# Optimization experiments

Measured on AMD Instinct MI355X. Metric: run time of the kernel, lower is better.

The kernel has to match this reference:

```python
import jax, jax.numpy as jnp
import numpy as np

NT, NGRID, NX, HID, NY = 365, 1000, 20, 256, 1


def setup_inputs() -> dict:
    key = jax.random.key(0)
    ks = jax.random.split(key, 10)
    s_in = 1.0 / np.sqrt(NX)
    s_h = 1.0 / np.sqrt(HID)
    inp = {
        "x": jax.random.normal(ks[0], (NT, NGRID, NX), dtype=jnp.float32),
        "wt_ih": jnp.zeros((4 * HID, HID), dtype=jnp.float32),
        "W_in": jax.random.uniform(ks[1], (HID, NX), jnp.float32, -s_in, s_in),
        "b_in": jax.random.uniform(ks[2], (HID,), jnp.float32, -s_in, s_in),
        "W_ih": jax.random.uniform(ks[3], (4 * HID, HID), jnp.float32, -s_h, s_h),
        "W_hh": jax.random.uniform(ks[4], (4 * HID, HID), jnp.float32, -s_h, s_h),
        "b_ih": jax.random.uniform(ks[5], (4 * HID,), jnp.float32, -s_h, s_h),
        "b_hh": jax.random.uniform(ks[6], (4 * HID,), jnp.float32, -s_h, s_h),
        "W_out": jax.random.uniform(ks[7], (NY, HID), jnp.float32, -s_h, s_h),
        "b_out": jax.random.uniform(ks[8], (NY,), jnp.float32, -s_h, s_h),
    }
    return inp


def _lstm_forward(x, W_in, b_in, W_ih, W_hh, b_ih, b_hh, W_out, b_out):
    # linearIn + ReLU: [nt, ngrid, hid]
    x0 = jax.nn.relu(jnp.einsum("tnx,hx->tnh", x, W_in) + b_in)
    # precompute input contribution to gates for all timesteps: [nt, ngrid, 4*hid]
    gx = jnp.einsum("tnh,gh->tng", x0, W_ih) + b_ih + b_hh
    h0 = jnp.zeros((x.shape[1], HID), dtype=x.dtype)
    c0 = jnp.zeros((x.shape[1], HID), dtype=x.dtype)

    def step(carry, gx_t):
        h, c = carry
        gates = gx_t + h @ W_hh.T  # [ngrid, 4*hid]
        i, f, g, o = jnp.split(gates, 4, axis=-1)  # torch LSTMCell gate order
        i = jax.nn.sigmoid(i)
        f = jax.nn.sigmoid(f)
        g = jnp.tanh(g)
        o = jax.nn.sigmoid(o)
        c_new = f * c + i * g
        h_new = o * jnp.tanh(c_new)
        return (h_new, c_new), h_new

    _, hs = jax.lax.scan(step, (h0, c0), gx)  # hs: [nt, ngrid, hid]
    return jnp.einsum("tnh,yh->tny", hs, W_out) + b_out


def reference(x, wt_ih, W_in, b_in, W_ih, W_hh, b_ih, b_hh, W_out, b_out):
    # wt_ih only perturbs weights in training mode (and is zero here); eval-mode math:
    return _lstm_forward(x, W_in, b_in, W_ih, W_hh, b_ih, b_hh, W_out, b_out)
```

## Files before the change

### kernel.cpp

```cpp
#include <hip/hip_runtime.h>
#include <hip/hip_fp16.h>

#define NT    365
#define NGRID 1000
#define NXI   20
#define HID   256
#define GATES 1024
#define MROWS 365000
#define MBLK  5704
#define MPAD  (MBLK * 64)
#define NCL   63
#define CPTS  16
#define HX_TOT ((size_t)NT * NCL * 1024)
#define HX_ZERO ((size_t)NCL * 1024)

typedef _Float16 half8 __attribute__((ext_vector_type(8)));
typedef float floatx4 __attribute__((ext_vector_type(4)));
typedef unsigned long long u64;

#define SENT 0xFFFFFFFFFFFFFFFFull

__device__ _Float16 g_gx[(size_t)MPAD * GATES];
__device__ _Float16 g_wif[64 * 8 * 512];
__device__ _Float16 g_whf[2 * 32 * 8 * 64 * 8];
__device__ u64 g_hx[HX_TOT];

__device__ __forceinline__ float fsig(float x) {
  return __fdividef(1.f, 1.f + __expf(-x));
}
__device__ __forceinline__ float ftanh(float x) {
  return 1.f - __fdividef(2.f, __expf(2.f * x) + 1.f);
}

__global__ __launch_bounds__(256) void pack_wf_kernel(
    const float* __restrict__ W_ih, const float* __restrict__ W_hh) {
  const int gid = blockIdx.x * 256 + threadIdx.x;
  const float* src;
  _Float16* dst;
  int n, k0, lane;
  if (gid < 32768) {
    const int tile = gid >> 9;
    const int ks   = (gid >> 6) & 7;
    lane = gid & 63;
    n  = tile * 16 + (lane & 15);
    k0 = ks * 32 + (lane >> 4) * 8;
    src = W_ih + n * HID + k0;
    dst = g_wif + ((size_t)(tile * 8 + ks) * 64 + lane) * 8;
  } else {
    const int rem = gid - 32768;
    const int b2  = rem >> 14;
    const int lt  = (rem >> 9) & 31;
    const int ks  = (rem >> 6) & 7;
    lane = rem & 63;
    const int nt = (lt >> 3) * 16 + b2 * 8 + (lt & 7);
    n  = nt * 16 + (lane & 15);
    k0 = ks * 32 + (lane >> 4) * 8;
    src = W_hh + n * HID + k0;
    dst = g_whf + ((size_t)((b2 * 32 + lt) * 8 + ks) * 64 + lane) * 8;
  }
  const float4 a = *(const float4*)(src);
  const float4 b = *(const float4*)(src + 4);
  half8 h;
  h[0] = (_Float16)a.x; h[1] = (_Float16)a.y; h[2] = (_Float16)a.z; h[3] = (_Float16)a.w;
  h[4] = (_Float16)b.x; h[5] = (_Float16)b.y; h[6] = (_Float16)b.z; h[7] = (_Float16)b.w;
  *(half8*)dst = h;
}

__global__ __launch_bounds__(256, 2) void gx_kernel(
    const float* __restrict__ x, const float* __restrict__ W_in,
    const float* __restrict__ b_in, const float* __restrict__ b_ih,
    const float* __restrict__ b_hh, float* __restrict__ y) {
  {
    const size_t gid = (size_t)blockIdx.x * 256 + threadIdx.x;
    const size_t TT  = (size_t)MBLK * 256;
    for (size_t j = gid; j < HX_TOT; j += TT)
      g_hx[j] = (j < HX_ZERO) ? 0ull : SENT;
    if (gid < MROWS) y[gid] = 0.f;
  }

  __shared__ float s_x[64 * NXI];
  __shared__ float s_bias[GATES];
  __shared__ _Float16 s_x0[64 * 264];
  __shared__ _Float16 s_out[64 * 264];

  const int tid  = threadIdx.x;
  const int lane = tid & 63;
  const int w    = tid >> 6;
  const int jg   = lane >> 4;
  const int m0   = blockIdx.x * 64;

  #pragma unroll
  for (int i = 0; i < 5; ++i) {
    const int idx = i * 256 + tid;
    size_t g = (size_t)m0 * NXI + idx;
    const size_t gmax = (size_t)MROWS * NXI - 1;
    if (g > gmax) g = gmax;
    s_x[idx] = x[g];
  }
  #pragma unroll
  for (int i = 0; i < 4; ++i) {
    const int g = i * 256 + tid;
    s_bias[g] = b_ih[g] + b_hh[g];
  }
  float wv[NXI];
  #pragma unroll
  for (int k = 0; k < NXI; ++k) wv[k] = W_in[tid * NXI + k];
  const float bv = b_in[tid];
  __syncthreads();

  half8 bf[4][4];
  #pragma unroll
  for (int p = 0; p < 4; ++p)
    #pragma unroll
    for (int ni = 0; ni < 4; ++ni)
      bf[p][ni] = *(const half8*)(g_wif +
          ((size_t)((w * 4 + ni) * 8 + p) * 64 + lane) * 8);

  for (int r = 0; r < 64; ++r) {
    float acc = bv;
    #pragma unroll
    for (int qq = 0; qq < 5; ++qq) {
      const float4 xa = *(const float4*)&s_x[r * NXI + qq * 4];
      acc += xa.x * wv[qq * 4 + 0] + xa.y * wv[qq * 4 + 1] +
             xa.z * wv[qq * 4 + 2] + xa.w * wv[qq * 4 + 3];
    }
    s_x0[r * 264 + tid] = (_Float16)fmaxf(acc, 0.f);
  }
  __syncthreads();

  for (int ng = 0; ng < 4; ++ng) {
    floatx4 acc[4][4];
    #pragma unroll
    for (int mi = 0; mi < 4; ++mi)
      #pragma unroll
      for (int ni = 0; ni < 4; ++ni) acc[mi][ni] = (floatx4){0.f, 0.f, 0.f, 0.f};

    #pragma unroll
    for (int ks = 0; ks < 8; ++ks) {
      half8 a[4];
      #pragma unroll
      for (int mi = 0; mi < 4; ++mi)
        a[mi] = *(const half8*)&s_x0[(mi * 16 + (lane & 15)) * 264 + ks * 32 + (lane >> 4) * 8];
      #pragma unroll
      for (int mi = 0; mi < 4; ++mi)
        #pragma unroll
        for (int ni = 0; ni < 4; ++ni)
          acc[mi][ni] = __builtin_amdgcn_mfma_f32_16x16x32_f16(bf[ks & 3][ni], a[mi], acc[mi][ni], 0, 0, 0);
      if (ks + 4 < 8) {
        #pragma unroll
        for (int ni = 0; ni < 4; ++ni)
          bf[ks & 3][ni] = *(const half8*)(g_wif +
              ((size_t)((ng * 16 + w * 4 + ni) * 8 + (ks + 4)) * 64 + lane) * 8);
      } else if (ng + 1 < 4) {
        #pragma unroll
        for (int ni = 0; ni < 4; ++ni)
          bf[ks & 3][ni] = *(const half8*)(g_wif +
              ((size_t)(((ng + 1) * 16 + w * 4 + ni) * 8 + (ks - 4)) * 64 + lane) * 8);
      }
    }

    #pragma unroll
    for (int ni = 0; ni < 4; ++ni) {
      const int gbase = ng * 256 + (w * 4 + ni) * 16 + jg * 4;
      const float4 bs = *(const float4*)&s_bias[gbase];
      const int colw = (w * 4 + ni) * 16 + jg * 4;
      #pragma unroll
      for (int mi = 0; mi < 4; ++mi) {
        union { _Float16 h[4]; u64 u; } pk;
        pk.h[0] = (_Float16)(acc[mi][ni][0] + bs.x);
        pk.h[1] = (_Float16)(acc[mi][ni][1] + bs.y);
        pk.h[2] = (_Float16)(acc[mi][ni][2] + bs.z);
        pk.h[3] = (_Float16)(acc[mi][ni][3] + bs.w);
        *(u64*)&s_out[(mi * 16 + (lane & 15)) * 264 + colw] = pk.u;
      }
    }
    __syncthreads();

    #pragma unroll
    for (int i = 0; i < 8; ++i) {
      const int cid = i * 256 + tid;
      const int row = cid >> 5;
      const int c8  = (cid & 31) * 8;
      const half8 v = *(const half8*)&s_out[row * 264 + c8];
      const int phi = ((c8 >> 7) & 1) * 512 + ng * 128 + (c8 & 127);
      *(half8*)(g_gx + (size_t)(m0 + row) * GATES + phi) = v;
    }
    __syncthreads();
  }
}

__global__ __launch_bounds__(256, 1) void rec_kernel(
    const float* __restrict__ W_out, const float* __restrict__ b_out,
    float* __restrict__ y) {
  __shared__ float s_g[4 * 16 * 132];
  __shared__ u64   s_h[2][1024];

  const int tid = threadIdx.x;
  const int l   = tid & 63;
  const int w   = tid >> 6;
  const int c   = blockIdx.x >> 1;
  const int b   = blockIdx.x & 1;
  const int pt  = l & 15;
  const int jg  = l >> 4;

  half8 wf[8][8];
  #pragma unroll
  for (int slot = 0; slot < 8; ++slot) {
    const int lt = (slot >> 1) * 8 + 2 * w + (slot & 1);
    #pragma unroll
    for (int kk = 0; kk < 4; ++kk) {
      wf[slot][kk] = *(const half8*)(g_whf +
          ((size_t)((b * 32 + lt) * 8 + (b * 4 + kk)) * 64 + l) * 8);
      wf[slot][4 + kk] = *(const half8*)(g_whf +
          ((size_t)((b * 32 + lt) * 8 + ((1 - b) * 4 + kk)) * 64 + l) * 8);
    }
  }

  float cs[8];
  float wo[8];
  #pragma unroll
  for (int j = 0; j < 8; ++j) {
    cs[j] = 0.f;
    wo[j] = W_out[b * 128 + 32 * w + jg * 8 + j];
  }
  const float bo_eff = (b == 0 && w == 0) ? b_out[0] : 0.f;
  const int n_pt  = c * CPTS + pt;
  const int rn_pt = (n_pt < NGRID) ? n_pt : (NGRID - 1);
  const int peer0 = (1 - b) * 4;

  for (int i = tid; i < 1024; i += 256) s_h[0][i] = 0ull;

  half8 gxr[4];
  {
    const _Float16* gsrc = g_gx + (size_t)rn_pt * GATES + b * 512 + 32 * w + jg * 8;
    #pragma unroll
    for (int off = 0; off < 4; ++off)
      gxr[off] = *(const half8*)(gsrc + off * 128);
  }
  __syncthreads();

  for (int t = 0; t < NT; ++t) {
    const int cur = t & 1, nxt = cur ^ 1;
    const bool hasnext = (t + 1 < NT);

    const u64* hsrc = g_hx + ((size_t)t * NCL + c) * 1024;
    u64 pv[8];
    #pragma unroll
    for (int kk = 0; kk < 4; ++kk) {
      pv[2 * kk]     = __hip_atomic_load(hsrc +       (peer0 + kk) * 64 + l,
                                         __ATOMIC_RELAXED, __HIP_MEMORY_SCOPE_AGENT);
      pv[2 * kk + 1] = __hip_atomic_load(hsrc + 512 + (peer0 + kk) * 64 + l,
                                         __ATOMIC_RELAXED, __HIP_MEMORY_SCOPE_AGENT);
    }

    floatx4 acc[8];
    #pragma unroll
    for (int i = 0; i < 8; ++i) acc[i] = (floatx4){0.f, 0.f, 0.f, 0.f};

    #pragma unroll
    for (int kk = 0; kk < 4; ++kk) {
      union { u64 u[2]; half8 h; } af;
      af.u[0] = s_h[cur][kk * 64 + l];
      af.u[1] = s_h[cur][512 + kk * 64 + l];
      #pragma unroll
      for (int i = 0; i < 8; ++i)
        acc[i] = __builtin_amdgcn_mfma_f32_16x16x32_f16(af.h, wf[i][kk], acc[i], 0, 0, 0);
    }

    {
      bool pending = false;
      #pragma unroll
      for (int k = 0; k < 8; ++k) pending |= (pv[k] == SENT);
      int tries = 0;
      while (pending && ++tries < (1 << 18)) {
        pending = false;
        #pragma unroll
        for (int kk = 0; kk < 4; ++kk) {
          if (pv[2 * kk] == SENT)
            pv[2 * kk] = __hip_atomic_load(hsrc + (peer0 + kk) * 64 + l,
                                           __ATOMIC_RELAXED, __HIP_MEMORY_SCOPE_AGENT);
          if (pv[2 * kk + 1] == SENT)
            pv[2 * kk + 1] = __hip_atomic_load(hsrc + 512 + (peer0 + kk) * 64 + l,
                                               __ATOMIC_RELAXED, __HIP_MEMORY_SCOPE_AGENT);
        }
        #pragma unroll
        for (int k = 0; k < 8; ++k) pending |= (pv[k] == SENT);
      }
    }

    __builtin_amdgcn_sched_barrier(0);
    half8 gn[4];
    if (hasnext) {
      const _Float16* gsrc = g_gx + ((size_t)(t + 1) * NGRID + rn_pt) * GATES
                           + b * 512 + 32 * w + jg * 8;
      #pragma unroll
      for (int off = 0; off < 4; ++off)
        gn[off] = *(const half8*)(gsrc + off * 128);
    }

    #pragma unroll
    for (int kk = 0; kk < 4; ++kk) {
      union { u64 u[2]; half8 h; } af;
      af.u[0] = pv[2 * kk];
      af.u[1] = pv[2 * kk + 1];
      #pragma unroll
      for (int i = 0; i < 8; ++i)
        acc[i] = __builtin_amdgcn_mfma_f32_16x16x32_f16(af.h, wf[i][4 + kk], acc[i], 0, 0, 0);
    }

    #pragma unroll
    for (int slot = 0; slot < 8; ++slot) {
      const int colw = (slot >> 1) * 32 + (slot & 1) * 16 + pt;
      #pragma unroll
      for (int r = 0; r < 4; ++r)
        s_g[w * 2112 + (jg * 4 + r) * 132 + colw] = acc[slot][r];
    }

    {
      const float* gp = &s_g[w * 2112 + pt * 132 + jg * 8];
      union { u64 u[2]; _Float16 h[8]; } pub;
      float yp = 0.f;
      #pragma unroll
      for (int j = 0; j < 8; ++j) {
        const float gi = gp[j]      + (float)gxr[0][j];
        const float gf = gp[32 + j] + (float)gxr[1][j];
        const float gg = gp[64 + j] + (float)gxr[2][j];
        const float go = gp[96 + j] + (float)gxr[3][j];
        const float i_ = fsig(gi);
        const float f_ = fsig(gf);
        const float g_ = ftanh(gg);
        const float o_ = fsig(go);
        cs[j] = f_ * cs[j] + i_ * g_;
        const float h = o_ * ftanh(cs[j]);
        pub.h[j] = (_Float16)h;
        yp += wo[j] * h;
      }
      if (hasnext) {
        u64* dst = g_hx + ((size_t)(t + 1) * NCL + c) * 1024 + (b * 4 + w) * 64 + l;
        __hip_atomic_store(dst,       pub.u[0], __ATOMIC_RELAXED, __HIP_MEMORY_SCOPE_AGENT);
        __hip_atomic_store(dst + 512, pub.u[1], __ATOMIC_RELAXED, __HIP_MEMORY_SCOPE_AGENT);
      }
      s_h[nxt][w * 64 + l]       = pub.u[0];
      s_h[nxt][512 + w * 64 + l] = pub.u[1];
      yp += __shfl_xor(yp, 16);
      yp += __shfl_xor(yp, 32);
      if (jg == 0 && n_pt < NGRID)
        atomicAdd(&y[(size_t)t * NGRID + n_pt], yp + bo_eff);
    }

    if (hasnext) {
      #pragma unroll
      for (int off = 0; off < 4; ++off) gxr[off] = gn[off];
    }

    __syncthreads();
  }
}

extern "C" void kernel_launch(void* const* d_in, const int* in_sizes, int n_in,
                              void* d_out, int out_size, void* d_ws, size_t ws_size,
                              hipStream_t stream) {
  (void)in_sizes; (void)n_in; (void)out_size; (void)d_ws; (void)ws_size;
  const float* x     = (const float*)d_in[0];
  const float* W_in  = (const float*)d_in[2];
  const float* b_in  = (const float*)d_in[3];
  const float* W_ih  = (const float*)d_in[4];
  const float* W_hh  = (const float*)d_in[5];
  const float* b_ih  = (const float*)d_in[6];
  const float* b_hh  = (const float*)d_in[7];
  const float* W_out = (const float*)d_in[8];
  const float* b_out = (const float*)d_in[9];
  float* y           = (float*)d_out;

  hipLaunchKernelGGL(pack_wf_kernel, dim3(256), dim3(256), 0, stream, W_ih, W_hh);
  hipLaunchKernelGGL(gx_kernel, dim3(MBLK), dim3(256), 0, stream,
                     x, W_in, b_in, b_ih, b_hh, y);
  hipLaunchKernelGGL(rec_kernel, dim3(NCL * 2), dim3(256), 0, stream, W_out, b_out, y);
}
```

Before: 1.703 ms.

## Swap MFMA operands so gate accumulators feed the LSTM cell directly

The recurrent MFMA operands are swapped (weights as A, hidden state as B), so each lane's accumulator already holds the gate values it needs for its own hidden units. The per-step spill of accumulators to shared memory (s_g) and the reload are removed. W_hh packing, W_out indexing and the gx loads are re-laid out to match the new column ownership: two 8-byte loads per gate instead of one 16-byte load. This shortens the serial per-timestep critical path, but the gx reads become narrower and are split into more load instructions.

```diff
diff --git a/kernel.cpp b/kernel.cpp
--- a/kernel.cpp
+++ b/kernel.cpp
@@ -35,31 +35,33 @@
 __global__ __launch_bounds__(256) void pack_wf_kernel(
     const float* __restrict__ W_ih, const float* __restrict__ W_hh) {
   const int gid = blockIdx.x * 256 + threadIdx.x;
-  const float* src;
+  const float* srcA;
+  const float* srcB;
   _Float16* dst;
-  int n, k0, lane;
   if (gid < 32768) {
     const int tile = gid >> 9;
     const int ks   = (gid >> 6) & 7;
-    lane = gid & 63;
-    n  = tile * 16 + (lane & 15);
-    k0 = ks * 32 + (lane >> 4) * 8;
-    src = W_ih + n * HID + k0;
+    const int lane = gid & 63;
+    const int n  = tile * 16 + (lane & 15);
+    const int k0 = ks * 32 + (lane >> 4) * 8;
+    srcA = W_ih + n * HID + k0;
+    srcB = srcA + 4;
     dst = g_wif + ((size_t)(tile * 8 + ks) * 64 + lane) * 8;
   } else {
     const int rem = gid - 32768;
     const int b2  = rem >> 14;
     const int lt  = (rem >> 9) & 31;
     const int ks  = (rem >> 6) & 7;
-    lane = rem & 63;
+    const int lane = rem & 63;
     const int nt = (lt >> 3) * 16 + b2 * 8 + (lt & 7);
-    n  = nt * 16 + (lane & 15);
-    k0 = ks * 32 + (lane >> 4) * 8;
-    src = W_hh + n * HID + k0;
+    const int n  = nt * 16 + (lane & 15);
+    const int k0 = ks * 32 + (lane >> 4) * 4;
+    srcA = W_hh + n * HID + k0;
+    srcB = W_hh + n * HID + k0 + 16;
     dst = g_whf + ((size_t)((b2 * 32 + lt) * 8 + ks) * 64 + lane) * 8;
   }
-  const float4 a = *(const float4*)(src);
-  const float4 b = *(const float4*)(src + 4);
+  const float4 a = *(const float4*)(srcA);
+  const float4 b = *(const float4*)(srcB);
   half8 h;
   h[0] = (_Float16)a.x; h[1] = (_Float16)a.y; h[2] = (_Float16)a.z; h[3] = (_Float16)a.w;
   h[4] = (_Float16)b.x; h[5] = (_Float16)b.y; h[6] = (_Float16)b.z; h[7] = (_Float16)b.w;
@@ -192,8 +194,7 @@
 __global__ __launch_bounds__(256, 1) void rec_kernel(
     const float* __restrict__ W_out, const float* __restrict__ b_out,
     float* __restrict__ y) {
-  __shared__ float s_g[4 * 16 * 132];
-  __shared__ u64   s_h[2][1024];
+  __shared__ u64 s_h[2][1024];
 
   const int tid = threadIdx.x;
   const int l   = tid & 63;
@@ -220,22 +221,28 @@
   float wo[8];
   #pragma unroll
   for (int j = 0; j < 8; ++j) {
+    const int d = (j < 4) ? (jg * 4 + j) : (16 + jg * 4 + (j - 4));
     cs[j] = 0.f;
-    wo[j] = W_out[b * 128 + 32 * w + jg * 8 + j];
+    wo[j] = W_out[b * 128 + 32 * w + d];
   }
   const float bo_eff = (b == 0 && w == 0) ? b_out[0] : 0.f;
   const int n_pt  = c * CPTS + pt;
   const int rn_pt = (n_pt < NGRID) ? n_pt : (NGRID - 1);
   const int peer0 = (1 - b) * 4;
+  const int gc0   = b * 512 + 32 * w + jg * 4;
 
   for (int i = tid; i < 1024; i += 256) s_h[0][i] = 0ull;
 
   half8 gxr[4];
   {
-    const _Float16* gsrc = g_gx + (size_t)rn_pt * GATES + b * 512 + 32 * w + jg * 8;
-    #pragma unroll
-    for (int off = 0; off < 4; ++off)
-      gxr[off] = *(const half8*)(gsrc + off * 128);
+    const _Float16* gb = g_gx + (size_t)rn_pt * GATES + gc0;
+    #pragma unroll
+    for (int off = 0; off < 4; ++off) {
+      union { u64 u[2]; half8 h; } gg;
+      gg.u[0] = *(const u64*)(gb + off * 128);
+      gg.u[1] = *(const u64*)(gb + off * 128 + 16);
+      gxr[off] = gg.h;
+    }
   }
   __syncthreads();
 
@@ -264,7 +271,7 @@
       af.u[1] = s_h[cur][512 + kk * 64 + l];
       #pragma unroll
       for (int i = 0; i < 8; ++i)
-        acc[i] = __builtin_amdgcn_mfma_f32_16x16x32_f16(af.h, wf[i][kk], acc[i], 0, 0, 0);
+        acc[i] = __builtin_amdgcn_mfma_f32_16x16x32_f16(wf[i][kk], af.h, acc[i], 0, 0, 0);
     }
 
     {
@@ -289,13 +296,14 @@
     }
 
     __builtin_amdgcn_sched_barrier(0);
-    half8 gn[4];
+    u64 gn[8];
     if (hasnext) {
-      const _Float16* gsrc = g_gx + ((size_t)(t + 1) * NGRID + rn_pt) * GATES
-                           + b * 512 + 32 * w + jg * 8;
-      #pragma unroll
-      for (int off = 0; off < 4; ++off)
-        gn[off] = *(const half8*)(gsrc + off * 128);
+      const _Float16* gb = g_gx + ((size_t)(t + 1) * NGRID + rn_pt) * GATES + gc0;
+      #pragma unroll
+      for (int off = 0; off < 4; ++off) {
+        gn[2 * off]     = *(const u64*)(gb + off * 128);
+        gn[2 * off + 1] = *(const u64*)(gb + off * 128 + 16);
+      }
     }
 
     #pragma unroll
@@ -305,27 +313,19 @@
       af.u[1] = pv[2 * kk + 1];
       #pragma unroll
       for (int i = 0; i < 8; ++i)
-        acc[i] = __builtin_amdgcn_mfma_f32_16x16x32_f16(af.h, wf[i][4 + kk], acc[i], 0, 0, 0);
-    }
-
-    #pragma unroll
-    for (int slot = 0; slot < 8; ++slot) {
-      const int colw = (slot >> 1) * 32 + (slot & 1) * 16 + pt;
-      #pragma unroll
-      for (int r = 0; r < 4; ++r)
-        s_g[w * 2112 + (jg * 4 + r) * 132 + colw] = acc[slot][r];
+        acc[i] = __builtin_amdgcn_mfma_f32_16x16x32_f16(wf[i][4 + kk], af.h, acc[i], 0, 0, 0);
     }
 
     {
-      const float* gp = &s_g[w * 2112 + pt * 132 + jg * 8];
       union { u64 u[2]; _Float16 h[8]; } pub;
       float yp = 0.f;
       #pragma unroll
       for (int j = 0; j < 8; ++j) {
-        const float gi = gp[j]      + (float)gxr[0][j];
-        const float gf = gp[32 + j] + (float)gxr[1][j];
-        const float gg = gp[64 + j] + (float)gxr[2][j];
-        const float go = gp[96 + j] + (float)gxr[3][j];
+        const int s = j >> 2, r = j & 3;
+        const float gi = acc[0 + s][r] + (float)gxr[0][j];
+        const float gf = acc[2 + s][r] + (float)gxr[1][j];
+        const float gg = acc[4 + s][r] + (float)gxr[2][j];
+        const float go = acc[6 + s][r] + (float)gxr[3][j];
         const float i_ = fsig(gi);
         const float f_ = fsig(gf);
         const float g_ = ftanh(gg);
@@ -350,7 +350,12 @@
 
     if (hasnext) {
       #pragma unroll
-      for (int off = 0; off < 4; ++off) gxr[off] = gn[off];
+      for (int off = 0; off < 4; ++off) {
+        union { u64 u[2]; half8 h; } gg;
+        gg.u[0] = gn[2 * off];
+        gg.u[1] = gn[2 * off + 1];
+        gxr[off] = gg.h;
+      }
     }
 
     __syncthreads();
```

After: 1.634 ms. -4.1%, faster.
